# Kernel tuning notes

Hardware: AMD Instinct MI355X
Metric: run time of the kernel (lower is better)

Reference implementation:

```python
import jax, jax.numpy as jnp
import numpy as np

HIDDEN = 1024
QKV = 1024
HEADS = 16
HEAD_DIM = QKV // HEADS
B, S = 4, 4096


def setup_inputs() -> dict:
    key = jax.random.key(0)
    ks = jax.random.split(key, 8)
    s = 1.0 / np.sqrt(HIDDEN)
    return {
        "x": jax.random.normal(ks[0], (B, S, HIDDEN), dtype=jnp.float32),
        "mask": jnp.ones((B, S, 1), dtype=jnp.float32),
        "Wq": jax.random.uniform(ks[1], (HIDDEN, QKV), jnp.float32, -s, s),
        "bq": jax.random.uniform(ks[2], (QKV,), jnp.float32, -s, s),
        "Wk": jax.random.uniform(ks[3], (HIDDEN, QKV), jnp.float32, -s, s),
        "bk": jax.random.uniform(ks[4], (QKV,), jnp.float32, -s, s),
        "Wv": jax.random.uniform(ks[5], (HIDDEN, QKV), jnp.float32, -s, s),
        "bv": jax.random.uniform(ks[6], (QKV,), jnp.float32, -s, s),
    }


def _split_heads(t):
    # [B, S, QKV] -> [B, H, S, D]
    b, s, _ = t.shape
    return t.reshape(b, s, HEADS, HEAD_DIM).transpose(0, 2, 1, 3)


def reference(x, mask, Wq, bq, Wk, bk, Wv, bv):
    q = (x @ Wq + bq) * mask  # [B, S, QKV]
    k = (x @ Wk + bk) * mask
    v = (x @ Wv + bv) * mask
    q, k, v = _split_heads(q), _split_heads(k), _split_heads(v)  # [B,H,S,D]
    # k^T @ v : [B, H, D, D]
    kv = jnp.einsum('bhsd,bhse->bhde', k, v)
    # per-batch norm constant from mask sum
    norm = mask.sum(axis=(-1, -2))  # [B]
    norm = 1.0 / jnp.sqrt(norm * HEAD_DIM)
    kv = kv * norm[:, None, None, None]
    # dropout is identity in eval mode
    out = jnp.einsum('bhsd,bhde->bhse', q, kv)  # [B, H, S, D]
    out = out.transpose(0, 2, 1, 3).reshape(B, S, QKV)
    return out
```

## Files before the change

kernel.cpp:

```cpp
#include <hip/hip_runtime.h>
#include <stdint.h>

#define HIDDEN 1024
#define SEQ 4096
#define BATCH 4
#define HEADS 16
#define HDIM 64
#define M_TOT (BATCH * SEQ)
#define NCH 4
#define NT 32

typedef __bf16 bf16x8 __attribute__((ext_vector_type(8)));
typedef float f32x4 __attribute__((ext_vector_type(4)));
typedef unsigned short u16x8 __attribute__((ext_vector_type(8)));

static __device__ __forceinline__ unsigned short f2bf(float f) {
  union { float f; uint32_t u; } v; v.f = f;
  uint32_t u = v.u;
  uint32_t r = (u + 0x7fffu + ((u >> 16) & 1u)) >> 16;
  return (unsigned short)r;
}
static __device__ __forceinline__ void load_lds16(const void* g, void* l) {
  __builtin_amdgcn_global_load_lds(
      (__attribute__((address_space(1))) void*)(g),
      (__attribute__((address_space(3))) void*)(l), 16, 0, 0);
}

__global__ __launch_bounds__(256) void prep_k(
    const float* __restrict__ x, unsigned short* __restrict__ xb,
    const float* __restrict__ Wk, const float* __restrict__ Wv,
    const float* __restrict__ Wq,
    unsigned short* __restrict__ Bt, unsigned short* __restrict__ Wqt,
    const float* __restrict__ bk, const float* __restrict__ bv,
    float* __restrict__ bkv,
    const float* __restrict__ mask, float* __restrict__ norm) {
  const int bid = blockIdx.x;
  const int tid = threadIdx.x;
  __shared__ float ts[64][65];
  if (bid < 8192) {
    int idx = bid * 256 + tid;
    const float4* xv = (const float4*)x;
    float4 a = xv[(size_t)idx * 2];
    float4 b = xv[(size_t)idx * 2 + 1];
    u16x8 o;
    o[0] = f2bf(a.x); o[1] = f2bf(a.y); o[2] = f2bf(a.z); o[3] = f2bf(a.w);
    o[4] = f2bf(b.x); o[5] = f2bf(b.y); o[6] = f2bf(b.z); o[7] = f2bf(b.w);
    *(u16x8*)(xb + (size_t)idx * 8) = o;
  } else if (bid < 8960) {
    int idx = bid - 8192;
    int z = idx >> 8, rem = idx & 255;
    const float* W = (z == 0) ? Wk : (z == 1) ? Wv : Wq;
    unsigned short* out = (z == 2) ? Wqt : (Bt + (size_t)z * HIDDEN * HIDDEN);
    int n0 = (rem & 15) * 64, k0 = (rem >> 4) * 64;
    int c = tid & 63, rq = tid >> 6;
    for (int i = 0; i < 16; ++i) {
      int r = i * 4 + rq;
      ts[r][c] = W[(size_t)(k0 + r) * HIDDEN + n0 + c];
    }
    __syncthreads();
    for (int i = 0; i < 16; ++i) {
      int n = i * 4 + rq;
      out[(size_t)(n0 + n) * HIDDEN + k0 + c] = f2bf(ts[c][n]);
    }
  } else if (bid < 8968) {
    int i = (bid - 8960) * 256 + tid;
    bkv[i] = (i < HIDDEN) ? bk[i] : bv[i - HIDDEN];
  } else {
    int b = bid - 8968;
    float s = 0.f;
    for (int i = tid; i < SEQ; i += 256) s += mask[b * SEQ + i];
    for (int off = 32; off; off >>= 1) s += __shfl_down(s, off);
    __shared__ float wsum[4];
    if ((tid & 63) == 0) wsum[tid >> 6] = s;
    __syncthreads();
    if (tid == 0) {
      float t = wsum[0] + wsum[1] + wsum[2] + wsum[3];
      norm[b] = rsqrtf(t * (float)HDIM);
    }
  }
}

template <int OUT_MODE>
__global__ __launch_bounds__(512, 4) void gemm256_k(
    const unsigned short* __restrict__ A, const unsigned short* __restrict__ Bt,
    const float* __restrict__ bias, const float* __restrict__ mask,
    const unsigned short* __restrict__ kvt,
    void* __restrict__ C, int nbn) {
  __shared__ unsigned short smem[32768];

  const int nwg = gridDim.x;
  const int bid = blockIdx.x;
  const int wg = (bid & 7) * (nwg >> 3) + (bid >> 3);
  const int row0 = (wg / nbn) * 256;
  const int col0 = (wg % nbn) * 128;

  const int tid = threadIdx.x;
  const int wave = tid >> 6;
  const int lane = tid & 63;
  const int wm = wave >> 1;
  const int wn = wave & 1;
  const int lr = lane & 15;
  const int hi = lane >> 4;

  const int srow = tid >> 2;
  const int sc = ((tid & 3) ^ ((srow >> 1) & 3)) * 8;
  const unsigned short* sA0 = A + (size_t)(row0 + srow) * HIDDEN + sc;
  const unsigned short* sA1 = A + (size_t)(row0 + 128 + srow) * HIDDEN + sc;
  const unsigned short* sB0 = Bt + (size_t)(col0 + srow) * HIDDEN + sc;

#define STAGE_A(tt) { int dst_ = ((tt) & 1) * 12288 + tid * 8; \
    load_lds16(sA0 + (size_t)(tt) * 32, &smem[dst_]); \
    load_lds16(sA1 + (size_t)(tt) * 32, &smem[dst_ + 4096]); }
#define STAGE_B(tt) { int dst_ = ((tt) & 1) * 12288 + 8192 + tid * 8; \
    load_lds16(sB0 + (size_t)(tt) * 32, &smem[dst_]); }

  const int kch = (hi ^ ((lr >> 1) & 3)) * 8;
  const int aoff = (wm * 64 + lr) * 32;
  const int boff = 8192 + (wn * 64 + lr) * 32;

  f32x4 acc[4][4];
#pragma unroll
  for (int i = 0; i < 4; ++i)
#pragma unroll
    for (int j = 0; j < 4; ++j) acc[i][j] = (f32x4){0.f, 0.f, 0.f, 0.f};

  STAGE_A(0) STAGE_B(0)
  asm volatile("s_waitcnt vmcnt(0)" ::: "memory");
  __builtin_amdgcn_s_barrier();

  for (int t = 0; t < NT; ++t) {
    const int bb = (t & 1) * 12288;
    if (t + 1 < NT) { STAGE_A(t + 1) STAGE_B(t + 1) }
    bf16x8 af[4], bf[4];
#pragma unroll
    for (int rf = 0; rf < 4; ++rf)
      af[rf] = *(const bf16x8*)&smem[bb + aoff + rf * 512 + kch];
#pragma unroll
    for (int cf = 0; cf < 4; ++cf)
      bf[cf] = *(const bf16x8*)&smem[bb + boff + cf * 512 + kch];
    __builtin_amdgcn_s_setprio(1);
#pragma unroll
    for (int rf = 0; rf < 4; ++rf)
#pragma unroll
      for (int cf = 0; cf < 4; ++cf)
        acc[rf][cf] = __builtin_amdgcn_mfma_f32_16x16x32_bf16(af[rf], bf[cf], acc[rf][cf], 0, 0, 0);
    __builtin_amdgcn_s_setprio(0);
    asm volatile("s_waitcnt vmcnt(0)" ::: "memory");
    __builtin_amdgcn_s_barrier();
  }

  float bcol[4];
#pragma unroll
  for (int cf = 0; cf < 4; ++cf)
    bcol[cf] = bias[col0 + wn * 64 + cf * 16 + lr];

  unsigned short* wt = &smem[wave * 4096];

  if (OUT_MODE == 2) {
    const int b = row0 >> 12;
    const int s0 = (row0 & 4095) + wm * 64;
    unsigned short* KVt = (unsigned short*)C;
#pragma unroll
    for (int rf = 0; rf < 4; ++rf)
#pragma unroll
      for (int j = 0; j < 4; ++j) {
        int r = rf * 16 + hi * 4 + j;
        float mrow = mask[row0 + wm * 64 + r];
#pragma unroll
        for (int cf = 0; cf < 4; ++cf) {
          int c = cf * 16 + lr;
          wt[c * 64 + (r ^ ((c & 7) << 3))] = f2bf((acc[rf][cf][j] + bcol[cf]) * mrow);
        }
      }
    asm volatile("s_waitcnt lgkmcnt(0)" ::: "memory");
#pragma unroll
    for (int i = 0; i < 8; ++i) {
      int flat = i * 64 + lane;
      int c = flat >> 3, rq = flat & 7;
      uint4 vv = *(const uint4*)&wt[c * 64 + ((rq * 8) ^ ((c & 7) << 3))];
      *(uint4*)&KVt[((size_t)(col0 + wn * 64 + c) * 4 + b) * 4096 + s0 + rq * 8] = vv;
    }
    asm volatile("s_waitcnt lgkmcnt(0)" ::: "memory");
  } else {
    float* Og = (float*)C;
    const int b = row0 >> 12;
    const int bh = b * 16 + (col0 >> 6) + wn;
    bf16x8 kvf[4][2];
#pragma unroll
    for (int et = 0; et < 4; ++et) {
      kvf[et][0] = *(const bf16x8*)&kvt[(size_t)bh * 4096 + (et * 16 + lr) * 64 + hi * 8];
      kvf[et][1] = *(const bf16x8*)&kvt[(size_t)bh * 4096 + (et * 16 + lr) * 64 + 32 + hi * 8];
    }
#pragma unroll
    for (int rf = 0; rf < 4; ++rf)
#pragma unroll
      for (int j = 0; j < 4; ++j) {
        int r = rf * 16 + hi * 4 + j;
        float mrow = mask[row0 + wm * 64 + r];
#pragma unroll
        for (int cf = 0; cf < 4; ++cf) {
          int c = cf * 16 + lr;
          wt[r * 64 + (c ^ ((r & 7) << 3))] = f2bf((acc[rf][cf][j] + bcol[cf]) * mrow);
        }
      }
    asm volatile("s_waitcnt lgkmcnt(0)" ::: "memory");
    const int echunk0 = (hi ^ (lr & 7)) * 8;
    const int echunk1 = ((4 + hi) ^ (lr & 7)) * 8;
#pragma unroll
    for (int g = 0; g < 4; ++g) {
      bf16x8 a0 = *(const bf16x8*)&wt[(g * 16 + lr) * 64 + echunk0];
      bf16x8 a1 = *(const bf16x8*)&wt[(g * 16 + lr) * 64 + echunk1];
#pragma unroll
      for (int et = 0; et < 4; ++et) {
        f32x4 o4 = (f32x4){0.f, 0.f, 0.f, 0.f};
        o4 = __builtin_amdgcn_mfma_f32_16x16x32_bf16(a0, kvf[et][0], o4, 0, 0, 0);
        o4 = __builtin_amdgcn_mfma_f32_16x16x32_bf16(a1, kvf[et][1], o4, 0, 0, 0);
#pragma unroll
        for (int j = 0; j < 4; ++j)
          __builtin_nontemporal_store(o4[j],
              &Og[(size_t)(row0 + wm * 64 + g * 16 + hi * 4 + j) * 1024
                  + col0 + wn * 64 + et * 16 + lr]);
      }
    }
    asm volatile("s_waitcnt lgkmcnt(0)" ::: "memory");
  }
#undef STAGE_A
#undef STAGE_B
}

__global__ __launch_bounds__(256) void kvpart2_k(const unsigned short* __restrict__ KVt,
                                                 float* __restrict__ part) {
  const int bh = blockIdx.x, ch = blockIdx.y;
  const int b = bh >> 4, h = bh & 15;
  __shared__ unsigned short tl[32768];
  const int tid = threadIdx.x;
  const int wave = tid >> 6, lane = tid & 63;
  const int lr = lane & 15, hi = lane >> 4;

  const int r0 = tid >> 3;
  const int cc0 = ((tid & 7) ^ (r0 & 7)) * 8;
  const int r1 = 32 + r0;
  const int cc1 = ((tid & 7) ^ (r1 & 7)) * 8;
  const unsigned short* A0 = KVt + ((size_t)(h * 64 + r0) * 4 + b) * 4096 + ch * 1024 + cc0;
  const unsigned short* A1 = KVt + ((size_t)(h * 64 + r1) * 4 + b) * 4096 + ch * 1024 + cc1;
  const unsigned short* B0 = KVt + ((size_t)(1024 + h * 64 + r0) * 4 + b) * 4096 + ch * 1024 + cc0;
  const unsigned short* B1 = KVt + ((size_t)(1024 + h * 64 + r1) * 4 + b) * 4096 + ch * 1024 + cc1;

#define KSTAGE(tt) { int bb2 = ((tt) & 3) * 8192; \
    load_lds16(A0 + (tt) * 64, &tl[bb2 + tid * 8]); \
    load_lds16(A1 + (tt) * 64, &tl[bb2 + 2048 + tid * 8]); \
    load_lds16(B0 + (tt) * 64, &tl[bb2 + 4096 + tid * 8]); \
    load_lds16(B1 + (tt) * 64, &tl[bb2 + 6144 + tid * 8]); }

  const int ra = wave * 16 + lr;
  const int aoff = ra * 64;
  const int ach0 = (hi ^ (ra & 7)) * 8, ach1 = ((4 + hi) ^ (ra & 7)) * 8;

  f32x4 acc4[4];
#pragma unroll
  for (int nt = 0; nt < 4; ++nt) acc4[nt] = (f32x4){0.f, 0.f, 0.f, 0.f};

  KSTAGE(0) KSTAGE(1)
  asm volatile("s_waitcnt vmcnt(4)" ::: "memory");
  __builtin_amdgcn_s_barrier();
  for (int t = 0; t < 16; ++t) {
    const int bb = (t & 3) * 8192;
    if (t + 2 < 16) KSTAGE(t + 2)
    bf16x8 a0 = *(const bf16x8*)&tl[bb + aoff + ach0];
    bf16x8 a1 = *(const bf16x8*)&tl[bb + aoff + ach1];
    bf16x8 bf0[4], bf1[4];
#pragma unroll
    for (int nt = 0; nt < 4; ++nt) {
      int rb = nt * 16 + lr;
      bf0[nt] = *(const bf16x8*)&tl[bb + 4096 + rb * 64 + ((hi ^ (rb & 7)) * 8)];
      bf1[nt] = *(const bf16x8*)&tl[bb + 4096 + rb * 64 + (((4 + hi) ^ (rb & 7)) * 8)];
    }
#pragma unroll
    for (int nt = 0; nt < 4; ++nt) {
      acc4[nt] = __builtin_amdgcn_mfma_f32_16x16x32_bf16(a0, bf0[nt], acc4[nt], 0, 0, 0);
      acc4[nt] = __builtin_amdgcn_mfma_f32_16x16x32_bf16(a1, bf1[nt], acc4[nt], 0, 0, 0);
    }
    if (t < 14) asm volatile("s_waitcnt vmcnt(4)" ::: "memory");
    else        asm volatile("s_waitcnt vmcnt(0)" ::: "memory");
    __builtin_amdgcn_s_barrier();
  }
  float* dst = part + ((size_t)(ch * 64 + bh)) * 4096;
#pragma unroll
  for (int nt = 0; nt < 4; ++nt)
#pragma unroll
    for (int j = 0; j < 4; ++j)
      dst[(wave * 16 + hi * 4 + j) * 64 + nt * 16 + lr] = acc4[nt][j];
#undef KSTAGE
}

__global__ void kvreduce_k(const float* __restrict__ part, const float* __restrict__ norm,
                           unsigned short* __restrict__ kvt) {
  int idx4 = (blockIdx.x * 256 + threadIdx.x) * 4;
  int bh = idx4 >> 12, rem = idx4 & 4095;
  int e = rem >> 6, d0 = rem & 63;
  float s0 = 0.f, s1 = 0.f, s2 = 0.f, s3 = 0.f;
#pragma unroll
  for (int ch = 0; ch < NCH; ++ch) {
    const float* p = part + ((size_t)(ch * 64 + bh)) * 4096 + e;
    s0 += p[(d0 + 0) * 64];
    s1 += p[(d0 + 1) * 64];
    s2 += p[(d0 + 2) * 64];
    s3 += p[(d0 + 3) * 64];
  }
  float nb = norm[bh >> 4];
  ushort4 o;
  o.x = f2bf(s0 * nb); o.y = f2bf(s1 * nb); o.z = f2bf(s2 * nb); o.w = f2bf(s3 * nb);
  *(ushort4*)&kvt[idx4] = o;
}

extern "C" void kernel_launch(void* const* d_in, const int* in_sizes, int n_in,
                              void* d_out, int out_size, void* d_ws, size_t ws_size,
                              hipStream_t stream) {
  const float* x = (const float*)d_in[0];
  const float* mask = (const float*)d_in[1];
  const float* Wq = (const float*)d_in[2];
  const float* bq = (const float*)d_in[3];
  const float* Wk = (const float*)d_in[4];
  const float* bk = (const float*)d_in[5];
  const float* Wv = (const float*)d_in[6];
  const float* bv = (const float*)d_in[7];
  float* out = (float*)d_out;

  char* w = (char*)d_ws;
  unsigned short* xb = (unsigned short*)w;   w += (size_t)M_TOT * HIDDEN * 2;
  unsigned short* Bt = (unsigned short*)w;   w += (size_t)2048 * HIDDEN * 2;
  unsigned short* Wqt = (unsigned short*)w;  w += (size_t)HIDDEN * HIDDEN * 2;
  unsigned short* KVt = (unsigned short*)w;  w += (size_t)2048 * BATCH * SEQ * 2;
  float* part = (float*)w;                   w += (size_t)NCH * 64 * 4096 * 4;
  unsigned short* kvt = (unsigned short*)w;  w += (size_t)64 * 4096 * 2;
  float* bkv = (float*)w;                    w += 2048 * 4;
  float* norm = (float*)w;                   w += 64;

  prep_k<<<dim3(8972), dim3(256), 0, stream>>>(x, xb, Wk, Wv, Wq, Bt, Wqt, bk, bv, bkv, mask, norm);
  gemm256_k<2><<<dim3(1024), dim3(512), 0, stream>>>(xb, Bt, bkv, mask, nullptr, (void*)KVt, 16);
  kvpart2_k<<<dim3(64, NCH), dim3(256), 0, stream>>>(KVt, part);
  kvreduce_k<<<dim3(256), dim3(256), 0, stream>>>(part, norm, kvt);
  gemm256_k<4><<<dim3(512), dim3(512), 0, stream>>>(xb, Wqt, bq, mask, kvt, (void*)out, 8);
}
```

Baseline: 168.8 us.

## Shrink GEMM tile to 128x128 and load B fragments directly into registers

The projection GEMM tile shrinks from 256x128 with 512 threads to 128x128 with 256 threads, and each K step grows from 32 to 64. Only A is now staged through LDS. B fragments are read from global memory straight into double-buffered registers, alternating between two register sets across an unrolled pair of iterations. The goal is to cut LDS traffic and per-block LDS footprint, launch more blocks and halve the number of barriers. The cost is more redundant global and L2 reads of B across waves and a smaller tile with less reuse per block.

```diff
diff --git a/kernel.cpp b/kernel.cpp
--- a/kernel.cpp
+++ b/kernel.cpp
@@ -8,7 +8,7 @@
 #define HDIM 64
 #define M_TOT (BATCH * SEQ)
 #define NCH 4
-#define NT 32
+#define NT 16
 
 typedef __bf16 bf16x8 __attribute__((ext_vector_type(8)));
 typedef float f32x4 __attribute__((ext_vector_type(4)));
@@ -81,17 +81,17 @@
 }
 
 template <int OUT_MODE>
-__global__ __launch_bounds__(512, 4) void gemm256_k(
+__global__ __launch_bounds__(256, 2) void gemm128_k(
     const unsigned short* __restrict__ A, const unsigned short* __restrict__ Bt,
     const float* __restrict__ bias, const float* __restrict__ mask,
     const unsigned short* __restrict__ kvt,
     void* __restrict__ C, int nbn) {
-  __shared__ unsigned short smem[32768];
+  __shared__ unsigned short smem[16384];
 
   const int nwg = gridDim.x;
   const int bid = blockIdx.x;
   const int wg = (bid & 7) * (nwg >> 3) + (bid >> 3);
-  const int row0 = (wg / nbn) * 256;
+  const int row0 = (wg / nbn) * 128;
   const int col0 = (wg % nbn) * 128;
 
   const int tid = threadIdx.x;
@@ -102,21 +102,25 @@
   const int lr = lane & 15;
   const int hi = lane >> 4;
 
-  const int srow = tid >> 2;
-  const int sc = ((tid & 3) ^ ((srow >> 1) & 3)) * 8;
-  const unsigned short* sA0 = A + (size_t)(row0 + srow) * HIDDEN + sc;
-  const unsigned short* sA1 = A + (size_t)(row0 + 128 + srow) * HIDDEN + sc;
-  const unsigned short* sB0 = Bt + (size_t)(col0 + srow) * HIDDEN + sc;
-
-#define STAGE_A(tt) { int dst_ = ((tt) & 1) * 12288 + tid * 8; \
-    load_lds16(sA0 + (size_t)(tt) * 32, &smem[dst_]); \
-    load_lds16(sA1 + (size_t)(tt) * 32, &smem[dst_ + 4096]); }
-#define STAGE_B(tt) { int dst_ = ((tt) & 1) * 12288 + 8192 + tid * 8; \
-    load_lds16(sB0 + (size_t)(tt) * 32, &smem[dst_]); }
-
-  const int kch = (hi ^ ((lr >> 1) & 3)) * 8;
-  const int aoff = (wm * 64 + lr) * 32;
-  const int boff = 8192 + (wn * 64 + lr) * 32;
+  const int sr = tid >> 3;
+  const int sc = ((tid & 7) ^ (sr & 7)) * 8;
+  const unsigned short* sA = A + (size_t)(row0 + sr) * HIDDEN + sc;
+
+#define STAGE_A(tt) { int dst_ = ((tt) & 1) * 8192 + tid * 8; \
+    const unsigned short* s_ = sA + (size_t)(tt) * 64; \
+    load_lds16(s_,                          &smem[dst_]); \
+    load_lds16(s_ + (size_t)32 * HIDDEN,    &smem[dst_ + 2048]); \
+    load_lds16(s_ + (size_t)64 * HIDDEN,    &smem[dst_ + 4096]); \
+    load_lds16(s_ + (size_t)96 * HIDDEN,    &smem[dst_ + 6144]); }
+
+  const int chunk0 = (hi ^ (lr & 7)) * 8;
+  const int chunk1 = ((4 + hi) ^ (lr & 7)) * 8;
+  const int aoff = (wm * 64 + lr) * 64;
+
+  const unsigned short* Brow[4];
+#pragma unroll
+  for (int cf = 0; cf < 4; ++cf)
+    Brow[cf] = Bt + (size_t)(col0 + wn * 64 + cf * 16 + lr) * HIDDEN + hi * 8;
 
   f32x4 acc[4][4];
 #pragma unroll
@@ -124,30 +128,49 @@
 #pragma unroll
     for (int j = 0; j < 4; ++j) acc[i][j] = (f32x4){0.f, 0.f, 0.f, 0.f};
 
-  STAGE_A(0) STAGE_B(0)
+  STAGE_A(0)
+  bf16x8 b0[4][2], b1[4][2];
+#pragma unroll
+  for (int cf = 0; cf < 4; ++cf) {
+    b0[cf][0] = *(const bf16x8*)&Brow[cf][0];
+    b0[cf][1] = *(const bf16x8*)&Brow[cf][32];
+  }
   asm volatile("s_waitcnt vmcnt(0)" ::: "memory");
   __builtin_amdgcn_s_barrier();
 
-  for (int t = 0; t < NT; ++t) {
-    const int bb = (t & 1) * 12288;
-    if (t + 1 < NT) { STAGE_A(t + 1) STAGE_B(t + 1) }
-    bf16x8 af[4], bf[4];
-#pragma unroll
-    for (int rf = 0; rf < 4; ++rf)
-      af[rf] = *(const bf16x8*)&smem[bb + aoff + rf * 512 + kch];
-#pragma unroll
-    for (int cf = 0; cf < 4; ++cf)
-      bf[cf] = *(const bf16x8*)&smem[bb + boff + cf * 512 + kch];
-    __builtin_amdgcn_s_setprio(1);
-#pragma unroll
-    for (int rf = 0; rf < 4; ++rf)
-#pragma unroll
-      for (int cf = 0; cf < 4; ++cf)
-        acc[rf][cf] = __builtin_amdgcn_mfma_f32_16x16x32_bf16(af[rf], bf[cf], acc[rf][cf], 0, 0, 0);
-    __builtin_amdgcn_s_setprio(0);
-    asm volatile("s_waitcnt vmcnt(0)" ::: "memory");
-    __builtin_amdgcn_s_barrier();
-  }
+#define BODY(T, BC, BN) { \
+    const int bb_ = ((T) & 1) * 8192; \
+    if ((T) + 1 < NT) STAGE_A((T) + 1) \
+    if ((T) + 1 < NT) { \
+      _Pragma("unroll") \
+      for (int cf = 0; cf < 4; ++cf) { \
+        BN[cf][0] = *(const bf16x8*)&Brow[cf][((T) + 1) * 64]; \
+        BN[cf][1] = *(const bf16x8*)&Brow[cf][((T) + 1) * 64 + 32]; \
+      } \
+    } \
+    bf16x8 af_[4][2]; \
+    _Pragma("unroll") \
+    for (int rf = 0; rf < 4; ++rf) { \
+      af_[rf][0] = *(const bf16x8*)&smem[bb_ + aoff + rf * 1024 + chunk0]; \
+      af_[rf][1] = *(const bf16x8*)&smem[bb_ + aoff + rf * 1024 + chunk1]; \
+    } \
+    __builtin_amdgcn_s_setprio(1); \
+    _Pragma("unroll") \
+    for (int rf = 0; rf < 4; ++rf) \
+      _Pragma("unroll") \
+      for (int cf = 0; cf < 4; ++cf) \
+        _Pragma("unroll") \
+        for (int kh = 0; kh < 2; ++kh) \
+          acc[rf][cf] = __builtin_amdgcn_mfma_f32_16x16x32_bf16(af_[rf][kh], BC[cf][kh], acc[rf][cf], 0, 0, 0); \
+    __builtin_amdgcn_s_setprio(0); \
+    asm volatile("s_waitcnt vmcnt(0)" ::: "memory"); \
+    __builtin_amdgcn_s_barrier(); }
+
+  for (int tp = 0; tp < NT / 2; ++tp) {
+    BODY(2 * tp, b0, b1)
+    BODY(2 * tp + 1, b1, b0)
+  }
+#undef BODY
 
   float bcol[4];
 #pragma unroll
@@ -225,7 +248,6 @@
     asm volatile("s_waitcnt lgkmcnt(0)" ::: "memory");
   }
 #undef STAGE_A
-#undef STAGE_B
 }
 
 __global__ __launch_bounds__(256) void kvpart2_k(const unsigned short* __restrict__ KVt,
@@ -337,8 +359,8 @@
   float* norm = (float*)w;                   w += 64;
 
   prep_k<<<dim3(8972), dim3(256), 0, stream>>>(x, xb, Wk, Wv, Wq, Bt, Wqt, bk, bv, bkv, mask, norm);
-  gemm256_k<2><<<dim3(1024), dim3(512), 0, stream>>>(xb, Bt, bkv, mask, nullptr, (void*)KVt, 16);
+  gemm128_k<2><<<dim3(2048), dim3(256), 0, stream>>>(xb, Bt, bkv, mask, nullptr, (void*)KVt, 16);
   kvpart2_k<<<dim3(64, NCH), dim3(256), 0, stream>>>(KVt, part);
   kvreduce_k<<<dim3(256), dim3(256), 0, stream>>>(part, norm, kvt);
-  gemm256_k<4><<<dim3(512), dim3(512), 0, stream>>>(xb, Wqt, bq, mask, kvt, (void*)out, 8);
-}
+  gemm128_k<4><<<dim3(1024), dim3(256), 0, stream>>>(xb, Wqt, bq, mask, kvt, (void*)out, 8);
+}
```

After: 264.3 us. +56.5%, slower.
